# Kernel tuning notes

Measured on AMD Instinct MI355X. Metric: run time of the kernel, lower is better.

## Reference

```python
import jax, jax.numpy as jnp
import numpy as np

G = 8   # channel groups
K = 4   # top-k per group


def setup_inputs() -> dict:
    key = jax.random.key(0)
    ks = jax.random.split(key, 6)
    B, C, H, W = 16, 256, 128, 128
    x = jax.random.normal(ks[0], (B, C, H, W), dtype=jnp.float32)
    # 1x1 conv weights (kernel dims squeezed):
    soft_w1 = jax.random.normal(ks[1], (G, C // G), dtype=jnp.float32) * 0.1  # grouped Conv2d(C, G, 1, groups=G)
    soft_w2 = jax.random.normal(ks[2], (C, G), dtype=jnp.float32) * 0.1       # Conv2d(G, C, 1)
    top_w1 = jax.random.normal(ks[3], (G, K), dtype=jnp.float32) * 0.1        # grouped Conv2d(G*K, G, 1, groups=G)
    top_w2 = jax.random.normal(ks[4], (C, G), dtype=jnp.float32) * 0.1        # Conv2d(G, C, 1)
    r = jax.random.normal(ks[5], (2,), dtype=jnp.float32)                     # branch mixing logits
    return {"x": x, "soft_w1": soft_w1, "soft_w2": soft_w2,
            "top_w1": top_w1, "top_w2": top_w2, "r": r}


def reference(x, soft_w1, soft_w2, top_w1, top_w2, r):
    B, C, H, W = x.shape
    Cg = C // G
    xg = x.reshape(B, G, Cg, H, W)

    # --- CGSoftmax branch: x + conv2(conv1(x * softmax_per_group(x))) ---
    att = jax.nn.softmax(xg, axis=2)          # softmax over within-group channels
    xs = xg * att                              # MulRes
    y = jnp.einsum('bgchw,gc->bghw', xs, soft_w1)     # grouped 1x1 conv C->G
    soft_out = x + jnp.einsum('bghw,og->bohw', y, soft_w2)  # 1x1 conv G->C, AddRes

    # --- CGTopK branch: x + conv2(conv1(topk_per_group(x))) ---
    tk = -jnp.sort(-xg, axis=2)[:, :, :K]      # top-K values, sorted descending: [B,G,K,H,W]
    yt = jnp.einsum('bgkhw,gk->bghw', tk, top_w1)     # grouped 1x1 conv G*K->G
    top_out = x + jnp.einsum('bghw,og->bohw', yt, top_w2)  # 1x1 conv G->C, AddRes

    # --- softmax-weighted branch combine ---
    w = jax.nn.softmax(r)
    rt, rs = w[0], w[1]
    return top_out * rt + soft_out * rs
```

## Files before the change

### kernel.cpp

```cpp
#include <hip/hip_runtime.h>
#include <math.h>


#define G_ 8
#define K_ 4
#define CG_ 32
#define C_ 256
#define HW_ (128 * 128)

typedef __attribute__((ext_vector_type(2))) float f32x2;
typedef __attribute__((ext_vector_type(4))) float f32x4;

static __device__ __forceinline__ f32x2 pk2(float s) { return f32x2{s, s}; }

static __device__ __forceinline__ f32x2 maxv(f32x2 a, f32x2 b) {
    return __builtin_elementwise_max(a, b);
}

static __device__ __forceinline__ f32x2 fmav(f32x2 a, f32x2 b, f32x2 c) {
    return __builtin_elementwise_fma(a, b, c);
}

static __device__ __forceinline__ f32x2 med3v(f32x2 u, f32x2 x, f32x2 y) {
    return f32x2{__builtin_amdgcn_fmed3f(u.x, x.x, y.x),
                 __builtin_amdgcn_fmed3f(u.y, x.y, y.y)};
}

__launch_bounds__(512, 4)
__global__ void cgblock_kernel(const float* __restrict__ x,
                               const float* __restrict__ soft_w1,
                               const float* __restrict__ soft_w2,
                               const float* __restrict__ top_w1,
                               const float* __restrict__ top_w2,
                               const float* __restrict__ r,
                               float* __restrict__ out) {
    __shared__ f32x4 Y[G_][64];

    const int lane = threadIdx.x & 63;
    const int g = __builtin_amdgcn_readfirstlane(threadIdx.x >> 6);
    const int blk = blockIdx.x;
    const int b = blk >> 7;
    const int s = ((blk & 127) << 7) | (lane << 1);

    const long base = (long)(b * C_ + g * CG_) * HW_ + s;
    const f32x2* xp = (const f32x2*)(x + base);

    const float e0 = __expf(r[0]);
    const float e1 = __expf(r[1]);
    const float rt = e0 / (e0 + e1);
    const float rs = e1 / (e0 + e1);

    f32x2 v[CG_];
#pragma unroll
    for (int c = 0; c < CG_; ++c) {
        v[c] = __builtin_nontemporal_load(xp + c * (HW_ / 2));
    }

    f32x2 mm[16];
#pragma unroll
    for (int i = 0; i < 16; ++i) mm[i] = maxv(v[i], v[i + 16]);
#pragma unroll
    for (int st = 8; st >= 1; st >>= 1) {
#pragma unroll
        for (int i = 0; i < st; ++i) mm[i] = maxv(mm[i], mm[i + st]);
    }
    const f32x2 m = mm[0];

    f32x2 Z = pk2(0.f), acc = pk2(0.f);
#pragma unroll
    for (int c = 0; c < CG_; ++c) {
        const float w1 = soft_w1[g * CG_ + c];
        const f32x2 d = v[c] - m;
        const f32x2 e = f32x2{__expf(d.x), __expf(d.y)};
        Z += e;
        acc = fmav(v[c] * e, pk2(w1), acc);
    }
    const f32x2 ys = f32x2{acc.x / Z.x, acc.y / Z.y};

    f32x2 A0 = pk2(-INFINITY), A1 = pk2(-INFINITY);
    f32x2 A2 = pk2(-INFINITY), A3 = pk2(-INFINITY);
#pragma unroll
    for (int c = 0; c < CG_; ++c) {
        const f32x2 u = v[c];
        const f32x2 n0 = maxv(A0, u);
        const f32x2 n1 = med3v(u, A0, A1);
        const f32x2 n2 = med3v(u, A1, A2);
        const f32x2 n3 = med3v(u, A2, A3);
        A0 = n0; A1 = n1; A2 = n2; A3 = n3;
    }
    const float tw0 = top_w1[g * K_ + 0], tw1 = top_w1[g * K_ + 1];
    const float tw2 = top_w1[g * K_ + 2], tw3 = top_w1[g * K_ + 3];
    f32x2 yt = A3 * pk2(tw3);
    yt = fmav(A2, pk2(tw2), yt);
    yt = fmav(A1, pk2(tw1), yt);
    yt = fmav(A0, pk2(tw0), yt);

    const f32x2 yss = ys * pk2(rs);
    const f32x2 ytt = yt * pk2(rt);
    Y[g][lane] = f32x4{yss.x, yss.y, ytt.x, ytt.y};
    __syncthreads();

    f32x4 yv[G_];
#pragma unroll
    for (int gg = 0; gg < G_; ++gg) yv[gg] = Y[gg][lane];

    f32x2* op = (f32x2*)(out + base);
    const float* w2s = soft_w2 + g * CG_ * G_;
    const float* w2t = top_w2 + g * CG_ * G_;
#pragma unroll
    for (int c = 0; c < CG_; ++c) {
        f32x2 o = v[c];
#pragma unroll
        for (int gg = 0; gg < G_; ++gg) {
            const float cs = w2s[c * G_ + gg];
            const float ct = w2t[c * G_ + gg];
            const f32x2 yf = f32x2{yv[gg].x, yv[gg].y};
            const f32x2 tf = f32x2{yv[gg].z, yv[gg].w};
            o = fmav(pk2(cs), yf, o);
            o = fmav(pk2(ct), tf, o);
        }
        __builtin_nontemporal_store(o, op + c * (HW_ / 2));
    }
}

extern "C" void kernel_launch(void* const* d_in, const int* in_sizes, int n_in,
                              void* d_out, int out_size, void* d_ws, size_t ws_size,
                              hipStream_t stream) {
    const float* x       = (const float*)d_in[0];
    const float* soft_w1 = (const float*)d_in[1];
    const float* soft_w2 = (const float*)d_in[2];
    const float* top_w1  = (const float*)d_in[3];
    const float* top_w2  = (const float*)d_in[4];
    const float* r       = (const float*)d_in[5];
    float* out = (float*)d_out;

    cgblock_kernel<<<dim3(2048), dim3(512), 0, stream>>>(
        x, soft_w1, soft_w2, top_w1, top_w2, r, out);
}
```

Measured before the change: 435.9 us.

## Make blocks persistent over four tiles with register double-buffered prefetch

Each block now processes four consecutive spatial tiles instead of one. While the current tile is computed, the next tile's 32 channel vectors are loaded into a second register array, and the LDS exchange buffer is double-buffered by tile parity. The aim is to overlap global-load latency with compute, and to amortise the per-block weight and softmax setup. In exchange it roughly doubles the registers spent on input data, lowers the occupancy target to 2 blocks, and launches only 512 blocks, which may not be enough parallelism to hide HBM latency in a kernel that is memory bound.

```diff
diff --git a/kernel.cpp b/kernel.cpp
--- a/kernel.cpp
+++ b/kernel.cpp
@@ -7,6 +7,8 @@
 #define CG_ 32
 #define C_ 256
 #define HW_ (128 * 128)
+#define TILES_ 4
+#define NBLK_ 512
 
 typedef __attribute__((ext_vector_type(2))) float f32x2;
 typedef __attribute__((ext_vector_type(4))) float f32x4;
@@ -26,39 +28,30 @@
                  __builtin_amdgcn_fmed3f(u.y, x.y, y.y)};
 }
 
-__launch_bounds__(512, 4)
-__global__ void cgblock_kernel(const float* __restrict__ x,
-                               const float* __restrict__ soft_w1,
-                               const float* __restrict__ soft_w2,
-                               const float* __restrict__ top_w1,
-                               const float* __restrict__ top_w2,
-                               const float* __restrict__ r,
-                               float* __restrict__ out) {
-    __shared__ f32x4 Y[G_][64];
+template <int PAR>
+static __device__ __forceinline__ void tile_body(
+    const float* __restrict__ x, float* __restrict__ out,
+    f32x2 (&vC)[CG_], f32x2 (&vN)[CG_], int tile, bool doLoad, int lane,
+    int g, const float* __restrict__ w1g, const float* __restrict__ w2s,
+    const float* __restrict__ w2t, float tw0, float tw1, float tw2,
+    float tw3, float rs, float rt, f32x4 (&Y)[2][G_][64]) {
+    const int b = tile >> 7;
+    const int s = ((tile & 127) << 7) | (lane << 1);
+    const long base = (long)(b * C_ + g * CG_) * HW_ + s;
 
-    const int lane = threadIdx.x & 63;
-    const int g = __builtin_amdgcn_readfirstlane(threadIdx.x >> 6);
-    const int blk = blockIdx.x;
-    const int b = blk >> 7;
-    const int s = ((blk & 127) << 7) | (lane << 1);
-
-    const long base = (long)(b * C_ + g * CG_) * HW_ + s;
-    const f32x2* xp = (const f32x2*)(x + base);
-
-    const float e0 = __expf(r[0]);
-    const float e1 = __expf(r[1]);
-    const float rt = e0 / (e0 + e1);
-    const float rs = e1 / (e0 + e1);
-
-    f32x2 v[CG_];
+    if (doLoad) {
+        const int nt = tile + 1;
+        const int nb = nt >> 7;
+        const int ns = ((nt & 127) << 7) | (lane << 1);
+        const f32x2* np = (const f32x2*)(x + (long)(nb * C_ + g * CG_) * HW_ + ns);
 #pragma unroll
-    for (int c = 0; c < CG_; ++c) {
-        v[c] = __builtin_nontemporal_load(xp + c * (HW_ / 2));
+        for (int c = 0; c < CG_; ++c)
+            vN[c] = __builtin_nontemporal_load(np + c * (HW_ / 2));
     }
 
     f32x2 mm[16];
 #pragma unroll
-    for (int i = 0; i < 16; ++i) mm[i] = maxv(v[i], v[i + 16]);
+    for (int i = 0; i < 16; ++i) mm[i] = maxv(vC[i], vC[i + 16]);
 #pragma unroll
     for (int st = 8; st >= 1; st >>= 1) {
 #pragma unroll
@@ -69,11 +62,11 @@
     f32x2 Z = pk2(0.f), acc = pk2(0.f);
 #pragma unroll
     for (int c = 0; c < CG_; ++c) {
-        const float w1 = soft_w1[g * CG_ + c];
-        const f32x2 d = v[c] - m;
+        const float w1 = w1g[c];
+        const f32x2 d = vC[c] - m;
         const f32x2 e = f32x2{__expf(d.x), __expf(d.y)};
         Z += e;
-        acc = fmav(v[c] * e, pk2(w1), acc);
+        acc = fmav(vC[c] * e, pk2(w1), acc);
     }
     const f32x2 ys = f32x2{acc.x / Z.x, acc.y / Z.y};
 
@@ -81,15 +74,13 @@
     f32x2 A2 = pk2(-INFINITY), A3 = pk2(-INFINITY);
 #pragma unroll
     for (int c = 0; c < CG_; ++c) {
-        const f32x2 u = v[c];
+        const f32x2 u = vC[c];
         const f32x2 n0 = maxv(A0, u);
         const f32x2 n1 = med3v(u, A0, A1);
         const f32x2 n2 = med3v(u, A1, A2);
         const f32x2 n3 = med3v(u, A2, A3);
         A0 = n0; A1 = n1; A2 = n2; A3 = n3;
     }
-    const float tw0 = top_w1[g * K_ + 0], tw1 = top_w1[g * K_ + 1];
-    const float tw2 = top_w1[g * K_ + 2], tw3 = top_w1[g * K_ + 3];
     f32x2 yt = A3 * pk2(tw3);
     yt = fmav(A2, pk2(tw2), yt);
     yt = fmav(A1, pk2(tw1), yt);
@@ -97,29 +88,70 @@
 
     const f32x2 yss = ys * pk2(rs);
     const f32x2 ytt = yt * pk2(rt);
-    Y[g][lane] = f32x4{yss.x, yss.y, ytt.x, ytt.y};
+    Y[PAR][g][lane] = f32x4{yss.x, yss.y, ytt.x, ytt.y};
     __syncthreads();
 
     f32x4 yv[G_];
 #pragma unroll
-    for (int gg = 0; gg < G_; ++gg) yv[gg] = Y[gg][lane];
+    for (int gg = 0; gg < G_; ++gg) yv[gg] = Y[PAR][gg][lane];
 
     f32x2* op = (f32x2*)(out + base);
-    const float* w2s = soft_w2 + g * CG_ * G_;
-    const float* w2t = top_w2 + g * CG_ * G_;
 #pragma unroll
     for (int c = 0; c < CG_; ++c) {
-        f32x2 o = v[c];
+        f32x2 o = vC[c];
 #pragma unroll
         for (int gg = 0; gg < G_; ++gg) {
             const float cs = w2s[c * G_ + gg];
             const float ct = w2t[c * G_ + gg];
-            const f32x2 yf = f32x2{yv[gg].x, yv[gg].y};
-            const f32x2 tf = f32x2{yv[gg].z, yv[gg].w};
-            o = fmav(pk2(cs), yf, o);
-            o = fmav(pk2(ct), tf, o);
+            o = fmav(pk2(cs), f32x2{yv[gg].x, yv[gg].y}, o);
+            o = fmav(pk2(ct), f32x2{yv[gg].z, yv[gg].w}, o);
         }
         __builtin_nontemporal_store(o, op + c * (HW_ / 2));
+    }
+}
+
+__launch_bounds__(512, 2)
+__global__ void cgblock_kernel(const float* __restrict__ x,
+                               const float* __restrict__ soft_w1,
+                               const float* __restrict__ soft_w2,
+                               const float* __restrict__ top_w1,
+                               const float* __restrict__ top_w2,
+                               const float* __restrict__ r,
+                               float* __restrict__ out) {
+    __shared__ f32x4 Y[2][G_][64];
+
+    const int lane = threadIdx.x & 63;
+    const int g = __builtin_amdgcn_readfirstlane(threadIdx.x >> 6);
+    const int tile0 = blockIdx.x * TILES_;
+
+    const float e0 = __expf(r[0]);
+    const float e1 = __expf(r[1]);
+    const float rt = e0 / (e0 + e1);
+    const float rs = e1 / (e0 + e1);
+
+    const float* w1g = soft_w1 + g * CG_;
+    const float* w2s = soft_w2 + g * CG_ * G_;
+    const float* w2t = top_w2 + g * CG_ * G_;
+    const float tw0 = top_w1[g * K_ + 0], tw1 = top_w1[g * K_ + 1];
+    const float tw2 = top_w1[g * K_ + 2], tw3 = top_w1[g * K_ + 3];
+
+    f32x2 vA[CG_], vB[CG_];
+
+    {
+        const int b = tile0 >> 7;
+        const int s = ((tile0 & 127) << 7) | (lane << 1);
+        const f32x2* xp = (const f32x2*)(x + (long)(b * C_ + g * CG_) * HW_ + s);
+#pragma unroll
+        for (int c = 0; c < CG_; ++c)
+            vA[c] = __builtin_nontemporal_load(xp + c * (HW_ / 2));
+    }
+
+#pragma unroll 1
+    for (int t = 0; t < TILES_; t += 2) {
+        tile_body<0>(x, out, vA, vB, tile0 + t, true, lane, g, w1g, w2s,
+                     w2t, tw0, tw1, tw2, tw3, rs, rt, Y);
+        tile_body<1>(x, out, vB, vA, tile0 + t + 1, (t + 2 < TILES_), lane,
+                     g, w1g, w2s, w2t, tw0, tw1, tw2, tw3, rs, rt, Y);
     }
 }
 
@@ -134,6 +166,6 @@
     const float* r       = (const float*)d_in[5];
     float* out = (float*)d_out;
 
-    cgblock_kernel<<<dim3(2048), dim3(512), 0, stream>>>(
+    cgblock_kernel<<<dim3(NBLK_), dim3(512), 0, stream>>>(
         x, soft_w1, soft_w2, top_w1, top_w2, r, out);
 }
```

Result: slower. 545.5 us (+25.2%).
